# Optimization experiments

Hardware: AMD Instinct MI355X
Metric: run time of the kernel (lower is better)

The kernel has to match this reference:

```python
import jax, jax.numpy as jnp
import numpy as np

B, T, D, H = 2, 2048, 768, 12
HS = D // H           # head_size = 64
FF = 4 * D            # feed_forward_multiplier = 4 -> hidden 3072
HALF = FF // 2        # SwiGLU halves hidden -> 1536
EPS = 1e-8


def rmsnorm(x, scale):
    # RMSNorm with p=-1: full-dim L2 norm / sqrt(d), then x/(rms+eps)*scale
    d = x.shape[-1]
    rms = jnp.linalg.norm(x, axis=-1, keepdims=True) * (d ** -0.5)
    return scale * (x / (rms + EPS))


def setup_inputs() -> dict:
    key = jax.random.key(0)
    ks = jax.random.split(key, 12)
    s = 0.02
    return {
        "x":  jax.random.normal(ks[0], (B, T, D), dtype=jnp.float32),
        "Wq": jax.random.normal(ks[1], (H, D, HS), dtype=jnp.float32) * s,
        "Wk": jax.random.normal(ks[2], (H, D, HS), dtype=jnp.float32) * s,
        "Wv": jax.random.normal(ks[3], (H, D, HS), dtype=jnp.float32) * s,
        "Wo": jax.random.normal(ks[4], (D, D), dtype=jnp.float32) * s,
        "bo": jnp.zeros((D,), dtype=jnp.float32),
        "W1": jax.random.normal(ks[5], (D, FF), dtype=jnp.float32) * s,
        "b1": jnp.zeros((FF,), dtype=jnp.float32),
        "W2": jax.random.normal(ks[6], (HALF, D), dtype=jnp.float32) * s,
        "b2": jnp.zeros((D,), dtype=jnp.float32),
        "g1": jnp.ones((D,), dtype=jnp.float32),
        "g2": jnp.ones((D,), dtype=jnp.float32),
    }


def reference(x, Wq, Wk, Wv, Wo, bo, W1, b1, W2, b2, g1, g2):
    Bx, Tx, Dx = x.shape
    # --- Multi-head causal attention (pre-RMSNorm, residual) ---
    h = rmsnorm(x, g1)
    q = jnp.einsum('btd,hdk->bhtk', h, Wq)
    k = jnp.einsum('btd,hdk->bhtk', h, Wk)
    v = jnp.einsum('btd,hdk->bhtk', h, Wv)
    # NOTE: original scales by C**-0.5 where C = embed_dim (not head_size)
    scores = jnp.einsum('bhtk,bhsk->bhts', q, k) * (Dx ** -0.5)
    causal = jnp.tril(jnp.ones((Tx, Tx), dtype=bool))
    scores = jnp.where(causal, scores, -jnp.inf)
    wei = jax.nn.softmax(scores, axis=-1)
    attn = jnp.einsum('bhts,bhsk->bhtk', wei, v)
    attn = attn.transpose(0, 2, 1, 3).reshape(Bx, Tx, Dx)  # concat heads
    x = x + attn @ Wo + bo
    # --- SwiGLU FFN (pre-RMSNorm, residual) ---
    h2 = rmsnorm(x, g2)
    u = h2 @ W1 + b1
    a, gate = jnp.split(u, 2, axis=-1)  # chunk: first half = value, second = gate
    x = x + (jax.nn.silu(gate) * a) @ W2 + b2
    return x
```

## Files before the change

kernel.cpp:

```cpp
#include <hip/hip_runtime.h>
#include <math.h>

#define TDIM 2048
#define DDIM 768
#define NH   12
#define NROWS 4096
#define EPSV 1e-8f
#define SCALE 0.03608439182435161f

typedef __bf16 bf16_t;
typedef bf16_t bf16x8 __attribute__((ext_vector_type(8)));
typedef bf16_t bf16x4 __attribute__((ext_vector_type(4)));
typedef float  floatx4 __attribute__((ext_vector_type(4)));

__device__ __forceinline__ void glds16(const bf16_t* g, bf16_t* l) {
    __builtin_amdgcn_global_load_lds(
        (const __attribute__((address_space(1))) void*)g,
        (__attribute__((address_space(3))) void*)l, 16, 0, 0);
}

__global__ __launch_bounds__(256) void pack_all(
    const float* __restrict__ Wq, const float* __restrict__ Wk,
    const float* __restrict__ Wv, const float* __restrict__ Wo,
    const float* __restrict__ W1, const float* __restrict__ W2,
    bf16_t* __restrict__ qkvw, bf16_t* __restrict__ wo,
    bf16_t* __restrict__ w1, bf16_t* __restrict__ w2)
{
    int bid = blockIdx.x;
    const float* src; bf16_t* dst;
    int srcld, dstld, k0, n0;
    if (bid < 144) {
        int kx = bid % 12, nx = bid / 12;
        src = Wo; dst = wo; srcld = 768; dstld = 768; k0 = kx * 64; n0 = nx * 64;
    } else if (bid < 720) {
        int t = bid - 144; int kx = t % 12, nx = t / 12;
        src = W1; dst = w1; srcld = 3072; dstld = 768; k0 = kx * 64; n0 = nx * 64;
    } else if (bid < 1008) {
        int t = bid - 720; int kx = t % 24, nx = t / 24;
        src = W2; dst = w2; srcld = 768; dstld = 1536; k0 = kx * 64; n0 = nx * 64;
    } else {
        int t = bid - 1008; int kx = t % 12, y = t / 12;
        int sel = y / 12, h = y - sel * 12;
        src = ((sel == 0) ? Wq : (sel == 1) ? Wk : Wv) + (size_t)h * 768 * 64;
        dst = qkvw + (size_t)(sel * 768 + h * 64) * 768;
        srcld = 64; dstld = 768; k0 = kx * 64; n0 = 0;
    }
    __shared__ float Ts[64][65];
    int tid = threadIdx.x;
    int r = tid >> 2, c = (tid & 3) * 16;
    const float* s = src + (size_t)(k0 + r) * srcld + n0 + c;
    #pragma unroll
    for (int i = 0; i < 4; i++) {
        float4 t = *(const float4*)(s + i * 4);
        Ts[r][c + i*4 + 0] = t.x; Ts[r][c + i*4 + 1] = t.y;
        Ts[r][c + i*4 + 2] = t.z; Ts[r][c + i*4 + 3] = t.w;
    }
    __syncthreads();
    int n = tid >> 2, kk = (tid & 3) * 16;
    bf16x8 o0, o1;
    #pragma unroll
    for (int i = 0; i < 8; i++) {
        o0[i] = (bf16_t)Ts[kk + i][n];
        o1[i] = (bf16_t)Ts[kk + 8 + i][n];
    }
    bf16_t* d = dst + (size_t)(n0 + n) * dstld + k0 + kk;
    *(bf16x8*)d = o0;
    *(bf16x8*)(d + 8) = o1;
}

__global__ __launch_bounds__(256) void rmsnorm_bf(
    const float* __restrict__ x, const float* __restrict__ g,
    bf16_t* __restrict__ out)
{
    int row = blockIdx.x;
    int tid = threadIdx.x;
    const float* xr = x + (size_t)row * DDIM;
    float v0 = xr[tid], v1 = xr[tid + 256], v2 = xr[tid + 512];
    float s = v0*v0 + v1*v1 + v2*v2;
    #pragma unroll
    for (int off = 32; off > 0; off >>= 1)
        s += __shfl_down(s, off, 64);
    __shared__ float red[4];
    __shared__ float tot;
    if ((tid & 63) == 0) red[tid >> 6] = s;
    __syncthreads();
    if (tid == 0) tot = red[0] + red[1] + red[2] + red[3];
    __syncthreads();
    float rms = sqrtf(tot * (1.0f / DDIM));
    float inv = 1.0f / (rms + EPSV);
    bf16_t* orow = out + (size_t)row * DDIM;
    orow[tid]       = (bf16_t)(g[tid]       * v0 * inv);
    orow[tid + 256] = (bf16_t)(g[tid + 256] * v1 * inv);
    orow[tid + 512] = (bf16_t)(g[tid + 512] * v2 * inv);
}

template<int TM>
__global__ __launch_bounds__(256) void gemm_bf16(
    const bf16_t* __restrict__ A, const bf16_t* __restrict__ BT, int K,
    float* __restrict__ Cf, bf16_t* __restrict__ Cb, int ldc,
    const float* __restrict__ bias, const float* __restrict__ resid)
{
    constexpr int MT = TM / 32;
    __shared__ bf16_t As0[TM][32], As1[TM][32];
    __shared__ bf16_t Bs0[128][32], Bs1[128][32];
    int tid = threadIdx.x;
    int wave = tid >> 6, lane = tid & 63;
    int lrow = lane & 15, quad = lane >> 4;
    int wm = wave >> 1, wn = wave & 1;

    int m0 = blockIdx.y * TM;
    int n0 = blockIdx.x * 128;

    int srow = lane >> 2, scol = (lane & 3) * 8;
    const bf16_t* Ag = A  + ((size_t)m0 + wave * (TM/4) + srow) * K + scol;
    const bf16_t* Bg = BT + ((size_t)n0 + wave * 32 + srow) * K + scol;

    floatx4 acc[MT][4];
    #pragma unroll
    for (int mt = 0; mt < MT; mt++)
        #pragma unroll
        for (int nt = 0; nt < 4; nt++)
            #pragma unroll
            for (int r = 0; r < 4; r++) acc[mt][nt][r] = 0.f;

    for (int k0 = 0; k0 < K; k0 += 64) {
        __syncthreads();
        #pragma unroll
        for (int i = 0; i < TM/64; i++) {
            glds16(Ag + (size_t)(i*16) * K + k0,      &As0[wave*(TM/4) + i*16][0]);
            glds16(Ag + (size_t)(i*16) * K + k0 + 32, &As1[wave*(TM/4) + i*16][0]);
        }
        #pragma unroll
        for (int i = 0; i < 2; i++) {
            glds16(Bg + (size_t)(i*16) * K + k0,      &Bs0[wave*32 + i*16][0]);
            glds16(Bg + (size_t)(i*16) * K + k0 + 32, &Bs1[wave*32 + i*16][0]);
        }
        __syncthreads();

        bf16x8 af0[MT], af1[MT], bf0[4], bf1[4];
        #pragma unroll
        for (int mt = 0; mt < MT; mt++) {
            af0[mt] = *(const bf16x8*)&As0[wm*(TM/2) + mt*16 + lrow][quad * 8];
            af1[mt] = *(const bf16x8*)&As1[wm*(TM/2) + mt*16 + lrow][quad * 8];
        }
        #pragma unroll
        for (int nt = 0; nt < 4; nt++) {
            bf0[nt] = *(const bf16x8*)&Bs0[wn*64 + nt*16 + lrow][quad * 8];
            bf1[nt] = *(const bf16x8*)&Bs1[wn*64 + nt*16 + lrow][quad * 8];
        }
        #pragma unroll
        for (int mt = 0; mt < MT; mt++)
            #pragma unroll
            for (int nt = 0; nt < 4; nt++) {
                acc[mt][nt] = __builtin_amdgcn_mfma_f32_16x16x32_bf16(
                    bf0[nt], af0[mt], acc[mt][nt], 0, 0, 0);
                acc[mt][nt] = __builtin_amdgcn_mfma_f32_16x16x32_bf16(
                    bf1[nt], af1[mt], acc[mt][nt], 0, 0, 0);
            }
    }

    int crow0 = m0 + wm * (TM/2);
    int ccol0 = n0 + wn * 64;
    #pragma unroll
    for (int mt = 0; mt < MT; mt++) {
        int row = crow0 + mt * 16 + lrow;
        #pragma unroll
        for (int nt = 0; nt < 4; nt++) {
            int col = ccol0 + nt * 16 + quad * 4;
            size_t off = (size_t)row * ldc + col;
            float4 bv = make_float4(0.f, 0.f, 0.f, 0.f);
            if (bias) bv = *(const float4*)(bias + col);
            float4 rs = make_float4(0.f, 0.f, 0.f, 0.f);
            if (resid) rs = *(const float4*)(resid + off);
            floatx4 a = acc[mt][nt];
            if (Cf) {
                float4 v;
                v.x = a[0] + bv.x + rs.x; v.y = a[1] + bv.y + rs.y;
                v.z = a[2] + bv.z + rs.z; v.w = a[3] + bv.w + rs.w;
                *(float4*)(Cf + off) = v;
            } else {
                bf16x4 v;
                v[0] = (bf16_t)(a[0] + bv.x + rs.x);
                v[1] = (bf16_t)(a[1] + bv.y + rs.y);
                v[2] = (bf16_t)(a[2] + bv.z + rs.z);
                v[3] = (bf16_t)(a[3] + bv.w + rs.w);
                *(bf16x4*)(Cb + off) = v;
            }
        }
    }
}

__global__ __launch_bounds__(256) void gemm_v(
    const bf16_t* __restrict__ A, const bf16_t* __restrict__ BT,
    bf16_t* __restrict__ vt)
{
    const int K = 768;
    __shared__ bf16_t As0[128][32], As1[128][32];
    __shared__ bf16_t Bs0[128][32], Bs1[128][32];
    int tid = threadIdx.x;
    int wave = tid >> 6, lane = tid & 63;
    int lrow = lane & 15, quad = lane >> 4;
    int wm = wave >> 1, wn = wave & 1;

    int m0 = blockIdx.y * 128;
    int n0 = blockIdx.x * 128;

    int srow = lane >> 2, scol = (lane & 3) * 8;
    const bf16_t* Ag = A  + ((size_t)m0 + wave * 32 + srow) * K + scol;
    const bf16_t* Bg = BT + ((size_t)n0 + wave * 32 + srow) * K + scol;

    floatx4 acc[4][4];
    #pragma unroll
    for (int mt = 0; mt < 4; mt++)
        #pragma unroll
        for (int nt = 0; nt < 4; nt++)
            #pragma unroll
            for (int r = 0; r < 4; r++) acc[mt][nt][r] = 0.f;

    for (int k0 = 0; k0 < K; k0 += 64) {
        __syncthreads();
        #pragma unroll
        for (int i = 0; i < 2; i++) {
            glds16(Ag + (size_t)(i*16) * K + k0,      &As0[wave*32 + i*16][0]);
            glds16(Ag + (size_t)(i*16) * K + k0 + 32, &As1[wave*32 + i*16][0]);
            glds16(Bg + (size_t)(i*16) * K + k0,      &Bs0[wave*32 + i*16][0]);
            glds16(Bg + (size_t)(i*16) * K + k0 + 32, &Bs1[wave*32 + i*16][0]);
        }
        __syncthreads();

        bf16x8 af0[4], af1[4], bf0[4], bf1[4];
        #pragma unroll
        for (int mt = 0; mt < 4; mt++) {
            af0[mt] = *(const bf16x8*)&As0[wm*64 + mt*16 + lrow][quad * 8];
            af1[mt] = *(const bf16x8*)&As1[wm*64 + mt*16 + lrow][quad * 8];
        }
        #pragma unroll
        for (int nt = 0; nt < 4; nt++) {
            bf0[nt] = *(const bf16x8*)&Bs0[wn*64 + nt*16 + lrow][quad * 8];
            bf1[nt] = *(const bf16x8*)&Bs1[wn*64 + nt*16 + lrow][quad * 8];
        }
        #pragma unroll
        for (int mt = 0; mt < 4; mt++)
            #pragma unroll
            for (int nt = 0; nt < 4; nt++) {
                acc[mt][nt] = __builtin_amdgcn_mfma_f32_16x16x32_bf16(
                    af0[mt], bf0[nt], acc[mt][nt], 0, 0, 0);
                acc[mt][nt] = __builtin_amdgcn_mfma_f32_16x16x32_bf16(
                    af1[mt], bf1[nt], acc[mt][nt], 0, 0, 0);
            }
    }

    #pragma unroll
    for (int nt = 0; nt < 4; nt++) {
        int d = n0 + wn * 64 + nt * 16 + lrow;
        int h = d >> 6, dl = d & 63;
        #pragma unroll
        for (int mt = 0; mt < 4; mt++) {
            int mg = m0 + wm * 64 + mt * 16 + quad * 4;
            int b = mg >> 11, tl = mg & 2047;
            bf16x4 v;
            #pragma unroll
            for (int r = 0; r < 4; r++) v[r] = (bf16_t)acc[mt][nt][r];
            *(bf16x4*)(vt + (((size_t)(b * NH + h) * 64 + dl) * TDIM + tl)) = v;
        }
    }
}

__global__ __launch_bounds__(256) void gemm_ffn1(
    const bf16_t* __restrict__ A, const bf16_t* __restrict__ W1t,
    const float* __restrict__ b1, bf16_t* __restrict__ sw)
{
    const int K = 768;
    __shared__ bf16_t As0[64][32], As1[64][32];
    __shared__ bf16_t Ba0[128][32], Ba1[128][32];
    __shared__ bf16_t Bg0[128][32], Bg1[128][32];
    int tid = threadIdx.x;
    int wave = tid >> 6, lane = tid & 63;
    int lrow = lane & 15, quad = lane >> 4;
    int wm = wave >> 1, wn = wave & 1;

    int m0 = blockIdx.y * 64;
    int n0 = blockIdx.x * 128;

    int srow = lane >> 2, scol = (lane & 3) * 8;
    const bf16_t* Agp = A   + ((size_t)m0 + wave * 16 + srow) * K + scol;
    const bf16_t* Bap = W1t + ((size_t)n0 + wave * 32 + srow) * K + scol;
    const bf16_t* Bgp = W1t + ((size_t)(1536 + n0) + wave * 32 + srow) * K + scol;

    floatx4 acc_a[2][4], acc_g[2][4];
    #pragma unroll
    for (int mt = 0; mt < 2; mt++)
        #pragma unroll
        for (int nt = 0; nt < 4; nt++)
            #pragma unroll
            for (int r = 0; r < 4; r++) { acc_a[mt][nt][r] = 0.f; acc_g[mt][nt][r] = 0.f; }

    for (int k0 = 0; k0 < K; k0 += 64) {
        __syncthreads();
        glds16(Agp + k0,      &As0[wave*16][0]);
        glds16(Agp + k0 + 32, &As1[wave*16][0]);
        #pragma unroll
        for (int i = 0; i < 2; i++) {
            glds16(Bap + (size_t)(i*16) * K + k0,      &Ba0[wave*32 + i*16][0]);
            glds16(Bap + (size_t)(i*16) * K + k0 + 32, &Ba1[wave*32 + i*16][0]);
            glds16(Bgp + (size_t)(i*16) * K + k0,      &Bg0[wave*32 + i*16][0]);
            glds16(Bgp + (size_t)(i*16) * K + k0 + 32, &Bg1[wave*32 + i*16][0]);
        }
        __syncthreads();

        bf16x8 af0[2], af1[2], ba0[4], ba1[4], bg0[4], bg1[4];
        #pragma unroll
        for (int mt = 0; mt < 2; mt++) {
            af0[mt] = *(const bf16x8*)&As0[wm*32 + mt*16 + lrow][quad * 8];
            af1[mt] = *(const bf16x8*)&As1[wm*32 + mt*16 + lrow][quad * 8];
        }
        #pragma unroll
        for (int nt = 0; nt < 4; nt++) {
            ba0[nt] = *(const bf16x8*)&Ba0[wn*64 + nt*16 + lrow][quad * 8];
            ba1[nt] = *(const bf16x8*)&Ba1[wn*64 + nt*16 + lrow][quad * 8];
            bg0[nt] = *(const bf16x8*)&Bg0[wn*64 + nt*16 + lrow][quad * 8];
            bg1[nt] = *(const bf16x8*)&Bg1[wn*64 + nt*16 + lrow][quad * 8];
        }
        #pragma unroll
        for (int mt = 0; mt < 2; mt++)
            #pragma unroll
            for (int nt = 0; nt < 4; nt++) {
                acc_a[mt][nt] = __builtin_amdgcn_mfma_f32_16x16x32_bf16(
                    ba0[nt], af0[mt], acc_a[mt][nt], 0, 0, 0);
                acc_a[mt][nt] = __builtin_amdgcn_mfma_f32_16x16x32_bf16(
                    ba1[nt], af1[mt], acc_a[mt][nt], 0, 0, 0);
                acc_g[mt][nt] = __builtin_amdgcn_mfma_f32_16x16x32_bf16(
                    bg0[nt], af0[mt], acc_g[mt][nt], 0, 0, 0);
                acc_g[mt][nt] = __builtin_amdgcn_mfma_f32_16x16x32_bf16(
                    bg1[nt], af1[mt], acc_g[mt][nt], 0, 0, 0);
            }
    }

    #pragma unroll
    for (int mt = 0; mt < 2; mt++) {
        int row = m0 + wm * 32 + mt * 16 + lrow;
        #pragma unroll
        for (int nt = 0; nt < 4; nt++) {
            int col = n0 + wn * 64 + nt * 16 + quad * 4;
            float4 bva = *(const float4*)(b1 + col);
            float4 bvg = *(const float4*)(b1 + 1536 + col);
            float av[4] = { acc_a[mt][nt][0] + bva.x, acc_a[mt][nt][1] + bva.y,
                            acc_a[mt][nt][2] + bva.z, acc_a[mt][nt][3] + bva.w };
            float gv[4] = { acc_g[mt][nt][0] + bvg.x, acc_g[mt][nt][1] + bvg.y,
                            acc_g[mt][nt][2] + bvg.z, acc_g[mt][nt][3] + bvg.w };
            bf16x4 v;
            #pragma unroll
            for (int r = 0; r < 4; r++)
                v[r] = (bf16_t)(av[r] * (gv[r] / (1.0f + __expf(-gv[r]))));
            *(bf16x4*)(sw + (size_t)row * 1536 + col) = v;
        }
    }
}

__global__ __launch_bounds__(256) void attn_mfma(
    const bf16_t* __restrict__ qk, const bf16_t* __restrict__ vt,
    bf16_t* __restrict__ o)
{
    const int QS = 1536;
    int bid = blockIdx.x;
    int p = bid >> 8, idx = bid & 255;
    int rank = (p == 1) ? (511 - idx) : (p * 256 + idx);
    int qt = 31 - rank / 24;
    int bh = rank % 24;
    int b = bh / NH, h = bh - b * NH;
    int tid = threadIdx.x;
    int wave = tid >> 6, lane = tid & 63;
    int lrow = lane & 15, quad = lane >> 4;

    __shared__ bf16_t Ks[64][72];
    __shared__ bf16_t Vt[64][72];
    __shared__ bf16_t Ps[4][16][72];

    size_t rbase = (size_t)b * TDIM;
    int q0 = qt * 64, qrow_w = q0 + wave * 16;

    const bf16_t* qp = qk + (rbase + qrow_w + lrow) * QS + h * 64;
    bf16x8 qf[2];
    qf[0] = *(const bf16x8*)(qp + quad * 8);
    qf[1] = *(const bf16x8*)(qp + 32 + quad * 8);

    floatx4 o_acc[4];
    #pragma unroll
    for (int mt = 0; mt < 4; mt++)
        #pragma unroll
        for (int r = 0; r < 4; r++) o_acc[mt][r] = 0.f;
    float m_r = -INFINITY, l_r = 0.f;

    int srow = tid >> 2;
    int scol = (tid & 3) * 16;

    for (int s = 0; s <= qt; s++) {
        __syncthreads();
        {
            const bf16_t* kp = qk + (rbase + s * 64 + srow) * QS + 768 + h * 64 + scol;
            *(bf16x8*)&Ks[srow][scol]     = *(const bf16x8*)kp;
            *(bf16x8*)&Ks[srow][scol + 8] = *(const bf16x8*)(kp + 8);
            const bf16_t* vp = vt + ((size_t)bh * 64 + srow) * TDIM + s * 64 + scol;
            *(bf16x8*)&Vt[srow][scol]     = *(const bf16x8*)vp;
            *(bf16x8*)&Vt[srow][scol + 8] = *(const bf16x8*)(vp + 8);
        }
        __syncthreads();

        floatx4 sfrag[4];
        #pragma unroll
        for (int nt = 0; nt < 4; nt++) {
            floatx4 a;
            #pragma unroll
            for (int r = 0; r < 4; r++) a[r] = 0.f;
            #pragma unroll
            for (int kf = 0; kf < 2; kf++) {
                bf16x8 afr = *(const bf16x8*)&Ks[nt * 16 + lrow][kf * 32 + quad * 8];
                a = __builtin_amdgcn_mfma_f32_16x16x32_bf16(afr, qf[kf], a, 0, 0, 0);
            }
            sfrag[nt] = a;
        }

        if (s == qt) {
            int qg = qrow_w + lrow;
            #pragma unroll
            for (int nt = 0; nt < 4; nt++)
                #pragma unroll
                for (int r = 0; r < 4; r++) {
                    int kc = s * 64 + nt * 16 + quad * 4 + r;
                    sfrag[nt][r] = (kc > qg) ? -INFINITY : sfrag[nt][r] * SCALE;
                }
        } else {
            #pragma unroll
            for (int nt = 0; nt < 4; nt++)
                #pragma unroll
                for (int r = 0; r < 4; r++) sfrag[nt][r] *= SCALE;
        }

        float mx = sfrag[0][0];
        #pragma unroll
        for (int nt = 0; nt < 4; nt++)
            #pragma unroll
            for (int r = 0; r < 4; r++) mx = fmaxf(mx, sfrag[nt][r]);
        mx = fmaxf(mx, __shfl_xor(mx, 16, 64));
        mx = fmaxf(mx, __shfl_xor(mx, 32, 64));
        float mn = fmaxf(m_r, mx);
        float alpha = __expf(m_r - mn);
        m_r = mn;

        float ls = 0.f;
        #pragma unroll
        for (int nt = 0; nt < 4; nt++) {
            bf16x4 pv;
            #pragma unroll
            for (int r = 0; r < 4; r++) {
                float p2 = __expf(sfrag[nt][r] - mn);
                ls += p2;
                pv[r] = (bf16_t)p2;
            }
            *(bf16x4*)&Ps[wave][lrow][nt * 16 + quad * 4] = pv;
        }
        ls += __shfl_xor(ls, 16, 64);
        ls += __shfl_xor(ls, 32, 64);
        l_r = l_r * alpha + ls;
        #pragma unroll
        for (int mt = 0; mt < 4; mt++)
            #pragma unroll
            for (int r = 0; r < 4; r++) o_acc[mt][r] *= alpha;

        #pragma unroll
        for (int kf = 0; kf < 2; kf++) {
            bf16x8 pfr = *(const bf16x8*)&Ps[wave][lrow][kf * 32 + quad * 8];
            #pragma unroll
            for (int mt = 0; mt < 4; mt++) {
                bf16x8 vfr = *(const bf16x8*)&Vt[mt * 16 + lrow][kf * 32 + quad * 8];
                o_acc[mt] = __builtin_amdgcn_mfma_f32_16x16x32_bf16(vfr, pfr, o_acc[mt], 0, 0, 0);
            }
        }
    }

    float inv = 1.0f / l_r;
    size_t rb = (rbase + qrow_w + lrow) * DDIM + h * 64;
    #pragma unroll
    for (int mt = 0; mt < 4; mt++) {
        bf16x4 ov;
        #pragma unroll
        for (int r = 0; r < 4; r++) ov[r] = (bf16_t)(o_acc[mt][r] * inv);
        *(bf16x4*)(o + rb + mt * 16 + quad * 4) = ov;
    }
}

extern "C" void kernel_launch(void* const* d_in, const int* in_sizes, int n_in,
                              void* d_out, int out_size, void* d_ws, size_t ws_size,
                              hipStream_t stream) {
    const float* x  = (const float*)d_in[0];
    const float* Wq = (const float*)d_in[1];
    const float* Wk = (const float*)d_in[2];
    const float* Wv = (const float*)d_in[3];
    const float* Wo = (const float*)d_in[4];
    const float* bo = (const float*)d_in[5];
    const float* W1 = (const float*)d_in[6];
    const float* b1 = (const float*)d_in[7];
    const float* W2 = (const float*)d_in[8];
    const float* b2 = (const float*)d_in[9];
    const float* g1 = (const float*)d_in[10];
    const float* g2 = (const float*)d_in[11];
    float* out = (float*)d_out;
    char* ws = (char*)d_ws;

    bf16_t* qkvw_bt = (bf16_t*)(ws);
    bf16_t* wo_bt   = (bf16_t*)(ws + 3538944);
    bf16_t* w1_bt   = (bf16_t*)(ws + 4718592);
    bf16_t* w2_bt   = (bf16_t*)(ws + 9437184);
    bf16_t* h_bf    = (bf16_t*)(ws + 11796480);
    bf16_t* qk      = (bf16_t*)(ws + 18087936);
    bf16_t* attn_bf = (bf16_t*)(ws + 30670848);
    bf16_t* sw_bf   = (bf16_t*)(ws + 36962304);
    bf16_t* vt      = (bf16_t*)(ws + 49545216);

    pack_all<<<1440, 256, 0, stream>>>(Wq, Wk, Wv, Wo, W1, W2,
                                       qkvw_bt, wo_bt, w1_bt, w2_bt);

    rmsnorm_bf<<<NROWS, 256, 0, stream>>>(x, g1, h_bf);

    gemm_bf16<128><<<dim3(12, 32), 256, 0, stream>>>(
        h_bf, qkvw_bt, 768, nullptr, qk, 1536, nullptr, nullptr);

    gemm_v<<<dim3(6, 32), 256, 0, stream>>>(h_bf, qkvw_bt + (size_t)1536 * 768, vt);

    attn_mfma<<<768, 256, 0, stream>>>(qk, vt, attn_bf);

    gemm_bf16<64><<<dim3(6, 64), 256, 0, stream>>>(
        attn_bf, wo_bt, 768, out, nullptr, 768, bo, x);

    rmsnorm_bf<<<NROWS, 256, 0, stream>>>(out, g2, h_bf);

    gemm_ffn1<<<dim3(12, 64), 256, 0, stream>>>(h_bf, w1_bt, b1, sw_bf);

    gemm_bf16<64><<<dim3(6, 64), 256, 0, stream>>>(
        sw_bf, w2_bt, 1536, out, nullptr, 768, b2, out);
}
```

Baseline: 269.9 us.

## Merge QK and V projections into one GEMM; use 128-row query tiles in attention

Fuses the QK projection GEMM and the V-transposed GEMM into a single launch: blocks with x index 12 and above write V in transposed layout, the rest write Q/K row-major. The attention kernel now handles 128 query rows per block, with each wave owning 32 rows, so every K/V tile loaded into shared memory serves twice as many queries. The grid drops from 768 to 384 blocks with a new causal load-balancing order. This removes one launch and halves K/V reloads, at the cost of more registers per wave and fewer blocks to fill the GPU.

```diff
diff --git a/kernel.cpp b/kernel.cpp
--- a/kernel.cpp
+++ b/kernel.cpp
@@ -190,9 +190,9 @@
     }
 }
 
-__global__ __launch_bounds__(256) void gemm_v(
-    const bf16_t* __restrict__ A, const bf16_t* __restrict__ BT,
-    bf16_t* __restrict__ vt)
+__global__ __launch_bounds__(256) void gemm_qkv(
+    const bf16_t* __restrict__ A, const bf16_t* __restrict__ QKVW,
+    bf16_t* __restrict__ qkout, bf16_t* __restrict__ vtout)
 {
     const int K = 768;
     __shared__ bf16_t As0[128][32], As1[128][32];
@@ -202,12 +202,14 @@
     int lrow = lane & 15, quad = lane >> 4;
     int wm = wave >> 1, wn = wave & 1;
 
+    int bx = blockIdx.x;
+    bool isV = (bx >= 12);
     int m0 = blockIdx.y * 128;
-    int n0 = blockIdx.x * 128;
+    int brow0 = isV ? 1536 + (bx - 12) * 128 : bx * 128;
 
     int srow = lane >> 2, scol = (lane & 3) * 8;
-    const bf16_t* Ag = A  + ((size_t)m0 + wave * 32 + srow) * K + scol;
-    const bf16_t* Bg = BT + ((size_t)n0 + wave * 32 + srow) * K + scol;
+    const bf16_t* Ag = A    + ((size_t)m0 + wave * 32 + srow) * K + scol;
+    const bf16_t* Bg = QKVW + ((size_t)brow0 + wave * 32 + srow) * K + scol;
 
     floatx4 acc[4][4];
     #pragma unroll
@@ -239,29 +241,58 @@
             bf0[nt] = *(const bf16x8*)&Bs0[wn*64 + nt*16 + lrow][quad * 8];
             bf1[nt] = *(const bf16x8*)&Bs1[wn*64 + nt*16 + lrow][quad * 8];
         }
-        #pragma unroll
-        for (int mt = 0; mt < 4; mt++)
+        if (!isV) {
+            #pragma unroll
+            for (int mt = 0; mt < 4; mt++)
+                #pragma unroll
+                for (int nt = 0; nt < 4; nt++) {
+                    acc[mt][nt] = __builtin_amdgcn_mfma_f32_16x16x32_bf16(
+                        bf0[nt], af0[mt], acc[mt][nt], 0, 0, 0);
+                    acc[mt][nt] = __builtin_amdgcn_mfma_f32_16x16x32_bf16(
+                        bf1[nt], af1[mt], acc[mt][nt], 0, 0, 0);
+                }
+        } else {
+            #pragma unroll
+            for (int mt = 0; mt < 4; mt++)
+                #pragma unroll
+                for (int nt = 0; nt < 4; nt++) {
+                    acc[mt][nt] = __builtin_amdgcn_mfma_f32_16x16x32_bf16(
+                        af0[mt], bf0[nt], acc[mt][nt], 0, 0, 0);
+                    acc[mt][nt] = __builtin_amdgcn_mfma_f32_16x16x32_bf16(
+                        af1[mt], bf1[nt], acc[mt][nt], 0, 0, 0);
+                }
+        }
+    }
+
+    if (!isV) {
+        int crow0 = m0 + wm * 64;
+        int ccol0 = brow0 + wn * 64;
+        #pragma unroll
+        for (int mt = 0; mt < 4; mt++) {
+            int row = crow0 + mt * 16 + lrow;
             #pragma unroll
             for (int nt = 0; nt < 4; nt++) {
-                acc[mt][nt] = __builtin_amdgcn_mfma_f32_16x16x32_bf16(
-                    af0[mt], bf0[nt], acc[mt][nt], 0, 0, 0);
-                acc[mt][nt] = __builtin_amdgcn_mfma_f32_16x16x32_bf16(
-                    af1[mt], bf1[nt], acc[mt][nt], 0, 0, 0);
-            }
-    }
-
-    #pragma unroll
-    for (int nt = 0; nt < 4; nt++) {
-        int d = n0 + wn * 64 + nt * 16 + lrow;
-        int h = d >> 6, dl = d & 63;
-        #pragma unroll
-        for (int mt = 0; mt < 4; mt++) {
-            int mg = m0 + wm * 64 + mt * 16 + quad * 4;
-            int b = mg >> 11, tl = mg & 2047;
-            bf16x4 v;
-            #pragma unroll
-            for (int r = 0; r < 4; r++) v[r] = (bf16_t)acc[mt][nt][r];
-            *(bf16x4*)(vt + (((size_t)(b * NH + h) * 64 + dl) * TDIM + tl)) = v;
+                int col = ccol0 + nt * 16 + quad * 4;
+                bf16x4 v;
+                #pragma unroll
+                for (int r = 0; r < 4; r++) v[r] = (bf16_t)acc[mt][nt][r];
+                *(bf16x4*)(qkout + (size_t)row * 1536 + col) = v;
+            }
+        }
+    } else {
+        #pragma unroll
+        for (int nt = 0; nt < 4; nt++) {
+            int d = (brow0 - 1536) + wn * 64 + nt * 16 + lrow;
+            int h = d >> 6, dl = d & 63;
+            #pragma unroll
+            for (int mt = 0; mt < 4; mt++) {
+                int mg = m0 + wm * 64 + mt * 16 + quad * 4;
+                int b = mg >> 11, tl = mg & 2047;
+                bf16x4 v;
+                #pragma unroll
+                for (int r = 0; r < 4; r++) v[r] = (bf16_t)acc[mt][nt][r];
+                *(bf16x4*)(vtout + (((size_t)(b * NH + h) * 64 + dl) * TDIM + tl)) = v;
+            }
         }
     }
 }
@@ -363,9 +394,8 @@
 {
     const int QS = 1536;
     int bid = blockIdx.x;
-    int p = bid >> 8, idx = bid & 255;
-    int rank = (p == 1) ? (511 - idx) : (p * 256 + idx);
-    int qt = 31 - rank / 24;
+    int rank = (bid < 256) ? bid : 639 - bid;
+    int qt = 15 - rank / 24;
     int bh = rank % 24;
     int b = bh / NH, h = bh - b * NH;
     int tid = threadIdx.x;
@@ -374,27 +404,34 @@
 
     __shared__ bf16_t Ks[64][72];
     __shared__ bf16_t Vt[64][72];
-    __shared__ bf16_t Ps[4][16][72];
+    __shared__ bf16_t Ps[4][32][72];
 
     size_t rbase = (size_t)b * TDIM;
-    int q0 = qt * 64, qrow_w = q0 + wave * 16;
-
-    const bf16_t* qp = qk + (rbase + qrow_w + lrow) * QS + h * 64;
-    bf16x8 qf[2];
-    qf[0] = *(const bf16x8*)(qp + quad * 8);
-    qf[1] = *(const bf16x8*)(qp + 32 + quad * 8);
-
-    floatx4 o_acc[4];
+    int q0 = qt * 128, qrow_w = q0 + wave * 32;
+
+    bf16x8 qf[2][2];
+    #pragma unroll
+    for (int nq = 0; nq < 2; nq++) {
+        const bf16_t* qp = qk + (rbase + qrow_w + nq * 16 + lrow) * QS + h * 64;
+        qf[0][nq] = *(const bf16x8*)(qp + quad * 8);
+        qf[1][nq] = *(const bf16x8*)(qp + 32 + quad * 8);
+    }
+
+    floatx4 o_acc[4][2];
     #pragma unroll
     for (int mt = 0; mt < 4; mt++)
         #pragma unroll
-        for (int r = 0; r < 4; r++) o_acc[mt][r] = 0.f;
-    float m_r = -INFINITY, l_r = 0.f;
+        for (int nq = 0; nq < 2; nq++)
+            #pragma unroll
+            for (int r = 0; r < 4; r++) o_acc[mt][nq][r] = 0.f;
+    float m_r[2] = {-INFINITY, -INFINITY};
+    float l_r[2] = {0.f, 0.f};
 
     int srow = tid >> 2;
     int scol = (tid & 3) * 16;
 
-    for (int s = 0; s <= qt; s++) {
+    int niter = 2 * qt + 2;
+    for (int s = 0; s < niter; s++) {
         __syncthreads();
         {
             const bf16_t* kp = qk + (rbase + s * 64 + srow) * QS + 768 + h * 64 + scol;
@@ -406,86 +443,99 @@
         }
         __syncthreads();
 
-        floatx4 sfrag[4];
-        #pragma unroll
-        for (int nt = 0; nt < 4; nt++) {
-            floatx4 a;
-            #pragma unroll
-            for (int r = 0; r < 4; r++) a[r] = 0.f;
-            #pragma unroll
-            for (int kf = 0; kf < 2; kf++) {
-                bf16x8 afr = *(const bf16x8*)&Ks[nt * 16 + lrow][kf * 32 + quad * 8];
-                a = __builtin_amdgcn_mfma_f32_16x16x32_bf16(afr, qf[kf], a, 0, 0, 0);
-            }
-            sfrag[nt] = a;
-        }
-
-        if (s == qt) {
-            int qg = qrow_w + lrow;
+        #pragma unroll
+        for (int nq = 0; nq < 2; nq++) {
+            floatx4 sfrag[4];
+            #pragma unroll
+            for (int nt = 0; nt < 4; nt++) {
+                floatx4 a;
+                #pragma unroll
+                for (int r = 0; r < 4; r++) a[r] = 0.f;
+                #pragma unroll
+                for (int kf = 0; kf < 2; kf++) {
+                    bf16x8 afr = *(const bf16x8*)&Ks[nt * 16 + lrow][kf * 32 + quad * 8];
+                    a = __builtin_amdgcn_mfma_f32_16x16x32_bf16(afr, qf[kf][nq], a, 0, 0, 0);
+                }
+                sfrag[nt] = a;
+            }
+
+            int qbase = qrow_w + nq * 16;
+            if (s * 64 + 63 > qbase) {
+                int qg = qbase + lrow;
+                #pragma unroll
+                for (int nt = 0; nt < 4; nt++)
+                    #pragma unroll
+                    for (int r = 0; r < 4; r++) {
+                        int kc = s * 64 + nt * 16 + quad * 4 + r;
+                        sfrag[nt][r] = (kc > qg) ? -INFINITY : sfrag[nt][r] * SCALE;
+                    }
+            } else {
+                #pragma unroll
+                for (int nt = 0; nt < 4; nt++)
+                    #pragma unroll
+                    for (int r = 0; r < 4; r++) sfrag[nt][r] *= SCALE;
+            }
+
+            float mx = sfrag[0][0];
             #pragma unroll
             for (int nt = 0; nt < 4; nt++)
                 #pragma unroll
+                for (int r = 0; r < 4; r++) mx = fmaxf(mx, sfrag[nt][r]);
+            mx = fmaxf(mx, __shfl_xor(mx, 16, 64));
+            mx = fmaxf(mx, __shfl_xor(mx, 32, 64));
+            float mn = fmaxf(m_r[nq], mx);
+            float alpha = __expf(m_r[nq] - mn);
+            m_r[nq] = mn;
+
+            float ls = 0.f;
+            #pragma unroll
+            for (int nt = 0; nt < 4; nt++) {
+                bf16x4 pv;
+                #pragma unroll
                 for (int r = 0; r < 4; r++) {
-                    int kc = s * 64 + nt * 16 + quad * 4 + r;
-                    sfrag[nt][r] = (kc > qg) ? -INFINITY : sfrag[nt][r] * SCALE;
+                    float p2 = __expf(sfrag[nt][r] - mn);
+                    ls += p2;
+                    pv[r] = (bf16_t)p2;
                 }
-        } else {
-            #pragma unroll
-            for (int nt = 0; nt < 4; nt++)
-                #pragma unroll
-                for (int r = 0; r < 4; r++) sfrag[nt][r] *= SCALE;
-        }
-
-        float mx = sfrag[0][0];
-        #pragma unroll
-        for (int nt = 0; nt < 4; nt++)
-            #pragma unroll
-            for (int r = 0; r < 4; r++) mx = fmaxf(mx, sfrag[nt][r]);
-        mx = fmaxf(mx, __shfl_xor(mx, 16, 64));
-        mx = fmaxf(mx, __shfl_xor(mx, 32, 64));
-        float mn = fmaxf(m_r, mx);
-        float alpha = __expf(m_r - mn);
-        m_r = mn;
-
-        float ls = 0.f;
-        #pragma unroll
-        for (int nt = 0; nt < 4; nt++) {
-            bf16x4 pv;
-            #pragma unroll
-            for (int r = 0; r < 4; r++) {
-                float p2 = __expf(sfrag[nt][r] - mn);
-                ls += p2;
-                pv[r] = (bf16_t)p2;
-            }
-            *(bf16x4*)&Ps[wave][lrow][nt * 16 + quad * 4] = pv;
-        }
-        ls += __shfl_xor(ls, 16, 64);
-        ls += __shfl_xor(ls, 32, 64);
-        l_r = l_r * alpha + ls;
-        #pragma unroll
-        for (int mt = 0; mt < 4; mt++)
-            #pragma unroll
-            for (int r = 0; r < 4; r++) o_acc[mt][r] *= alpha;
+                *(bf16x4*)&Ps[wave][nq * 16 + lrow][nt * 16 + quad * 4] = pv;
+            }
+            ls += __shfl_xor(ls, 16, 64);
+            ls += __shfl_xor(ls, 32, 64);
+            l_r[nq] = l_r[nq] * alpha + ls;
+            #pragma unroll
+            for (int mt = 0; mt < 4; mt++)
+                #pragma unroll
+                for (int r = 0; r < 4; r++) o_acc[mt][nq][r] *= alpha;
+        }
 
         #pragma unroll
         for (int kf = 0; kf < 2; kf++) {
-            bf16x8 pfr = *(const bf16x8*)&Ps[wave][lrow][kf * 32 + quad * 8];
+            bf16x8 pfr[2];
+            #pragma unroll
+            for (int nq = 0; nq < 2; nq++)
+                pfr[nq] = *(const bf16x8*)&Ps[wave][nq * 16 + lrow][kf * 32 + quad * 8];
             #pragma unroll
             for (int mt = 0; mt < 4; mt++) {
                 bf16x8 vfr = *(const bf16x8*)&Vt[mt * 16 + lrow][kf * 32 + quad * 8];
-                o_acc[mt] = __builtin_amdgcn_mfma_f32_16x16x32_bf16(vfr, pfr, o_acc[mt], 0, 0, 0);
-            }
-        }
-    }
-
-    float inv = 1.0f / l_r;
-    size_t rb = (rbase + qrow_w + lrow) * DDIM + h * 64;
-    #pragma unroll
-    for (int mt = 0; mt < 4; mt++) {
-        bf16x4 ov;
-        #pragma unroll
-        for (int r = 0; r < 4; r++) ov[r] = (bf16_t)(o_acc[mt][r] * inv);
-        *(bf16x4*)(o + rb + mt * 16 + quad * 4) = ov;
+                #pragma unroll
+                for (int nq = 0; nq < 2; nq++)
+                    o_acc[mt][nq] = __builtin_amdgcn_mfma_f32_16x16x32_bf16(
+                        vfr, pfr[nq], o_acc[mt][nq], 0, 0, 0);
+            }
+        }
+    }
+
+    #pragma unroll
+    for (int nq = 0; nq < 2; nq++) {
+        float inv = 1.0f / l_r[nq];
+        size_t rb = (rbase + qrow_w + nq * 16 + lrow) * DDIM + h * 64;
+        #pragma unroll
+        for (int mt = 0; mt < 4; mt++) {
+            bf16x4 ov;
+            #pragma unroll
+            for (int r = 0; r < 4; r++) ov[r] = (bf16_t)(o_acc[mt][nq][r] * inv);
+            *(bf16x4*)(o + rb + mt * 16 + quad * 4) = ov;
+        }
     }
 }
 
@@ -522,12 +572,9 @@
 
     rmsnorm_bf<<<NROWS, 256, 0, stream>>>(x, g1, h_bf);
 
-    gemm_bf16<128><<<dim3(12, 32), 256, 0, stream>>>(
-        h_bf, qkvw_bt, 768, nullptr, qk, 1536, nullptr, nullptr);
-
-    gemm_v<<<dim3(6, 32), 256, 0, stream>>>(h_bf, qkvw_bt + (size_t)1536 * 768, vt);
-
-    attn_mfma<<<768, 256, 0, stream>>>(qk, vt, attn_bf);
+    gemm_qkv<<<dim3(18, 32), 256, 0, stream>>>(h_bf, qkvw_bt, qk, vt);
+
+    attn_mfma<<<384, 256, 0, stream>>>(qk, vt, attn_bf);
 
     gemm_bf16<64><<<dim3(6, 64), 256, 0, stream>>>(
         attn_bf, wo_bt, 768, out, nullptr, 768, bo, x);
```

Result: slower. 290.3 us (+7.6%).
